# Performance work log

Measured on AMD Instinct MI355X. Metric: run time of the kernel, lower is better.

## Reference

```python
import jax, jax.numpy as jnp
import numpy as np

EPS = 1.1920929e-07  # torch.finfo(float32).eps, RMSNorm default eps

def _rms(x, w):
    return x * jax.lax.rsqrt(jnp.mean(x * x, axis=-1, keepdims=True) + EPS) * w

def setup_inputs() -> dict:
    key = jax.random.key(0)
    ks = jax.random.split(key, 8)
    V, E, M, L, B, T = 4096, 1024, 4096, 2, 32, 256
    s = 0.02
    return {
        "tokens": jax.random.randint(ks[0], (B, T), 0, V),
        "targets": jax.random.randint(ks[1], (B, T), 0, V),
        "emb_w": jax.random.normal(ks[2], (V, E), jnp.float32) * s,
        "block_norm_w": jax.random.normal(ks[3], (L, E), jnp.float32) * s,
        "fc1_w": jax.random.normal(ks[4], (L, M, E), jnp.float32) * s,
        "fc1_b": jnp.zeros((L, M), jnp.float32),
        "fc2_w": jax.random.normal(ks[5], (L, E, M), jnp.float32) * s,
        "fc2_b": jnp.zeros((L, E), jnp.float32),
        "norm_w": jax.random.normal(ks[6], (E,), jnp.float32) * s,
        "cur_w": jax.random.normal(ks[7], (E, E), jnp.float32) * s,
        "cur_b": jnp.zeros((E,), jnp.float32),
        "nxt_w": jax.random.normal(jax.random.fold_in(key, 99), (E, E), jnp.float32) * s,
        "nxt_b": jnp.zeros((E,), jnp.float32),
    }

def reference(tokens, targets, emb_w, block_norm_w, fc1_w, fc1_b, fc2_w, fc2_b,
              norm_w, cur_w, cur_b, nxt_w, nxt_b):
    B, T = tokens.shape
    E = emb_w.shape[1]
    L = block_norm_w.shape[0]
    embeds = emb_w[tokens]  # [B,T,E]

    def step(inp, xs):
        tok_emb, tok, tgt = xs  # [B,E], [B], [B]
        inp = tok_emb + inp
        h = inp
        for l in range(L):  # fixed small layer count
            y = jax.nn.silu(_rms(h, block_norm_w[l]) @ fc1_w[l].T + fc1_b[l])
            h = h + y @ fc2_w[l].T + fc2_b[l]
        x = _rms(inp + h, norm_w)
        cur_emb = x @ cur_w.T + cur_b
        nxt_emb = x @ nxt_w.T + nxt_b
        cur_logit = cur_emb @ emb_w.T  # [B,V]
        nxt_logit = nxt_emb @ emb_w.T
        lp_cur = jax.nn.log_softmax(cur_logit, axis=-1)
        lp_nxt = jax.nn.log_softmax(nxt_logit, axis=-1)
        ce_cur = -jnp.mean(jnp.take_along_axis(lp_cur, tok[:, None], axis=1))
        ce_nxt = -jnp.mean(jnp.take_along_axis(lp_nxt, tgt[:, None], axis=1))
        ce = (ce_cur + ce_nxt) / 2
        aux = jnp.mean((cur_emb - inp) ** 2)
        return nxt_emb, (nxt_logit, ce, aux)

    xs = (jnp.swapaxes(embeds, 0, 1), tokens.T, targets.T)
    init = jnp.zeros((B, E), embeds.dtype)
    _, (logits, ces, auxs) = jax.lax.scan(step, init, xs)
    return jnp.swapaxes(logits, 0, 1), jnp.mean(ces), jnp.mean(auxs)
```

## Files before the change

kernel.cpp:

```cpp
#include <hip/hip_runtime.h>
#include <math.h>

#define TT  256
#define BB  32
#define EE  1024
#define MM  4096
#define VV  4096
#define BE  (BB*EE)
#define NROWS (TT*BB)
#define EPSF 1.1920929e-07f

typedef _Float16 h2 __attribute__((ext_vector_type(2)));

__device__ inline float dot2f(h2 a, h2 b, float c) {
#if __has_builtin(__builtin_amdgcn_fdot2)
  return __builtin_amdgcn_fdot2(a, b, c, false);
#else
  return c + (float)a[0] * (float)b[0] + (float)a[1] * (float)b[1];
#endif
}

__device__ inline unsigned ldb_u32(const unsigned* p) {
  return __hip_atomic_load((unsigned*)p, __ATOMIC_RELAXED, __HIP_MEMORY_SCOPE_AGENT);
}
__device__ inline void stb_u32(unsigned* p, unsigned v) {
  __hip_atomic_store(p, v, __ATOMIC_RELAXED, __HIP_MEMORY_SCOPE_AGENT);
}
__device__ inline void stb_f32(float* p, float v) {
  __hip_atomic_store(p, v, __ATOMIC_RELAXED, __HIP_MEMORY_SCOPE_AGENT);
}

__device__ inline void gbar4(unsigned* cnt, int sidx) {
  __syncthreads();
  if (threadIdx.x == 0) {
    unsigned* base = cnt + (size_t)sidx * 17 * 32;
    unsigned* gp = base + (blockIdx.x & 15) * 32;
    unsigned* mp = base + 16 * 32;
    unsigned old = __hip_atomic_fetch_add(gp, 1u, __ATOMIC_RELAXED,
                                          __HIP_MEMORY_SCOPE_AGENT);
    if (old == 15u)
      __hip_atomic_fetch_add(mp, 1u, __ATOMIC_RELAXED, __HIP_MEMORY_SCOPE_AGENT);
    while (__hip_atomic_load(mp, __ATOMIC_RELAXED, __HIP_MEMORY_SCOPE_AGENT) < 16u)
      __builtin_amdgcn_s_sleep(1);
  }
  __syncthreads();
}

template<int NR>
__device__ float fc1like(int tid, int cu,
    const float* __restrict__ src, const float* __restrict__ scl,
    const h2* __restrict__ wl, h2* __restrict__ xs, float* __restrict__ red,
    float* __restrict__ ssrow,
    float* __restrict__ seedDst, const float* __restrict__ seedAdd,
    const float* __restrict__ seedBias) {
  const int b = tid & 31, kq = tid >> 5;
  const int sb = tid >> 4, se = (tid & 15) * 8;
  const int ep0 = (tid & 15) * 4;
  float ssacc = 0.f;
  float acc[NR];
#pragma unroll
  for (int m = 0; m < NR; ++m) acc[m] = 0.f;
  const int seedChunk = cu >> 5;
  const int seedOff = (cu & 1) * 4;
  const bool seeder = (seedDst != nullptr) && ((tid & 15) == ((cu & 31) >> 1));

  float4 v0, v1, c0v, c1v;
  auto ldchunk = [&](int c) {
    v0 = *(const float4*)&src[sb * EE + c * 128 + se];
    v1 = *(const float4*)&src[sb * EE + c * 128 + se + 4];
    c0v = *(const float4*)&scl[c * 128 + se];
    c1v = *(const float4*)&scl[c * 128 + se + 4];
  };
  auto flush = [&](int c) {
    h2* dst = xs + (c & 1) * (64 * 33);
    ssacc += v0.x*v0.x + v0.y*v0.y + v0.z*v0.z + v0.w*v0.w
           + v1.x*v1.x + v1.y*v1.y + v1.z*v1.z + v1.w*v1.w;
    h2 p0, p1, p2, p3;
    p0[0]=(_Float16)(v0.x*c0v.x); p0[1]=(_Float16)(v0.y*c0v.y);
    p1[0]=(_Float16)(v0.z*c0v.z); p1[1]=(_Float16)(v0.w*c0v.w);
    p2[0]=(_Float16)(v1.x*c1v.x); p2[1]=(_Float16)(v1.y*c1v.y);
    p3[0]=(_Float16)(v1.z*c1v.z); p3[1]=(_Float16)(v1.w*c1v.w);
    dst[(ep0+0)*33+sb]=p0; dst[(ep0+1)*33+sb]=p1;
    dst[(ep0+2)*33+sb]=p2; dst[(ep0+3)*33+sb]=p3;
    if (seeder && c == seedChunk) {
      const int e0 = c * 128 + se + seedOff;
      float a0, a1, a2, a3;
      if (seedOff == 0) { a0 = v0.x; a1 = v0.y; a2 = v0.z; a3 = v0.w; }
      else              { a0 = v1.x; a1 = v1.y; a2 = v1.z; a3 = v1.w; }
      float d0 = a0 + seedBias[e0 + 0];
      float d1 = a1 + seedBias[e0 + 1];
      float d2 = a2 + seedBias[e0 + 2];
      float d3 = a3 + seedBias[e0 + 3];
      if (seedAdd) {
        d0 += seedAdd[sb * EE + e0 + 0];
        d1 += seedAdd[sb * EE + e0 + 1];
        d2 += seedAdd[sb * EE + e0 + 2];
        d3 += seedAdd[sb * EE + e0 + 3];
      }
      stb_f32(&seedDst[sb * EE + e0 + 0], d0);
      stb_f32(&seedDst[sb * EE + e0 + 1], d1);
      stb_f32(&seedDst[sb * EE + e0 + 2], d2);
      stb_f32(&seedDst[sb * EE + e0 + 3], d3);
    }
  };
  ldchunk(0); flush(0);
  __syncthreads();
  for (int c = 0; c < 8; ++c) {
    if (c < 7) ldchunk(c + 1);
    const h2* xb = xs + (c & 1) * (64 * 33);
    h2 x0 = xb[(kq*4+0)*33+b], x1 = xb[(kq*4+1)*33+b],
       x2 = xb[(kq*4+2)*33+b], x3 = xb[(kq*4+3)*33+b];
#pragma unroll
    for (int m = 0; m < NR; ++m) {
      const h2* wp = &wl[m * 512 + c * 64 + kq * 4];
      float a = acc[m];
      a = dot2f(x0, wp[0], a); a = dot2f(x1, wp[1], a);
      a = dot2f(x2, wp[2], a); a = dot2f(x3, wp[3], a);
      acc[m] = a;
    }
    if (c < 7) flush(c + 1);
    __syncthreads();
  }
  ssacc += __shfl_xor(ssacc, 8);
  ssacc += __shfl_xor(ssacc, 4);
  ssacc += __shfl_xor(ssacc, 2);
  ssacc += __shfl_xor(ssacc, 1);
  if ((tid & 15) == 0) ssrow[sb] = ssacc;
#pragma unroll
  for (int m = 0; m < NR; ++m) acc[m] += __shfl_xor(acc[m], 32);
  const int wv = tid >> 6, ln = tid & 63;
  if (ln < 32) {
#pragma unroll
    for (int m = 0; m < NR; ++m) red[wv * 544 + ln * 17 + m] = acc[m];
  }
  __syncthreads();
  float z = 0.f;
  if (tid < 32 * NR) {
    const int b2 = (NR == 16) ? (tid >> 4) : (tid >> 2);
    const int m2 = tid & (NR - 1);
#pragma unroll
    for (int w = 0; w < 8; ++w) z += red[w * 544 + b2 * 17 + m2];
  }
  return z;
}

__device__ float fc2like(int tid,
    const unsigned* __restrict__ ysrc,
    const h2* __restrict__ wl, h2* __restrict__ xs, float* __restrict__ red) {
  const int b = tid & 31, kq = tid >> 5;
  const int sb = tid >> 4;
  const int ep0 = (tid & 15) * 4;
  float acc[16];
#pragma unroll
  for (int m = 0; m < 16; ++m) acc[m] = 0.f;
  unsigned q0, q1, q2, q3;
  auto ldchunk = [&](int c) {
    const unsigned* sp = ysrc + (size_t)sb * (MM / 2) + c * 64 + ep0;
    q0 = ldb_u32(sp + 0); q1 = ldb_u32(sp + 1);
    q2 = ldb_u32(sp + 2); q3 = ldb_u32(sp + 3);
  };
  auto flush = [&](int c) {
    h2* dst = xs + (c & 1) * (64 * 33);
    dst[(ep0+0)*33+sb] = __builtin_bit_cast(h2, q0);
    dst[(ep0+1)*33+sb] = __builtin_bit_cast(h2, q1);
    dst[(ep0+2)*33+sb] = __builtin_bit_cast(h2, q2);
    dst[(ep0+3)*33+sb] = __builtin_bit_cast(h2, q3);
  };
  ldchunk(0); flush(0);
  __syncthreads();
  for (int c = 0; c < 8; ++c) {
    if (c < 7) ldchunk(c + 1);
    const h2* xb = xs + (c & 1) * (64 * 33);
    h2 x0 = xb[(kq*4+0)*33+b], x1 = xb[(kq*4+1)*33+b],
       x2 = xb[(kq*4+2)*33+b], x3 = xb[(kq*4+3)*33+b];
#pragma unroll
    for (int m = 0; m < 16; ++m) {
      const h2* wp = &wl[m * 512 + c * 64 + kq * 4];
      float a = acc[m];
      a = dot2f(x0, wp[0], a); a = dot2f(x1, wp[1], a);
      a = dot2f(x2, wp[2], a); a = dot2f(x3, wp[3], a);
      acc[m] = a;
    }
    if (c < 7) flush(c + 1);
    __syncthreads();
  }
#pragma unroll
  for (int m = 0; m < 16; ++m) acc[m] += __shfl_xor(acc[m], 32);
  const int wv = tid >> 6, ln = tid & 63;
  if (ln < 32) {
#pragma unroll
    for (int m = 0; m < 16; ++m) red[wv * 544 + ln * 17 + m] = acc[m];
  }
  __syncthreads();
  const int b2 = tid >> 4, m2 = tid & 15;
  float z = 0.f;
#pragma unroll
  for (int w = 0; w < 8; ++w) z += red[w * 544 + b2 * 17 + m2];
  return z;
}

struct Scan4Params {
  const int* tokens; const float* embw;
  const float* bnw; const float* fc1w; const float* fc1b;
  const float* fc2w; const float* fc2b;
  const float* nw; const float* nxtw; const float* nxtb;
  float* inp_all;
  float* s_all;
  float* hbuf_all;
  float* nxt_all;
  unsigned* yh;
  float* ssS;
  unsigned* cnt;
};

__global__ __launch_bounds__(512, 1) void k_scan4(Scan4Params p) {
  extern __shared__ __align__(16) char smem[];
  h2* w1a = (h2*)smem;
  h2* w1b = (h2*)(smem + 32768);
  h2* w2a = (h2*)(smem + 65536);
  h2* w2b = (h2*)(smem + 98304);
  h2* wn  = (h2*)(smem + 131072);
  h2* xs  = (h2*)(smem + 139264);
  float* red = (float*)(smem + 139264);
  float* ssrow = (float*)(smem + 156672);
  const int tid = threadIdx.x;
  const int cu = blockIdx.x;
  const int cg = cu & 63, ks = cu >> 6;

#pragma unroll 4
  for (int r = 0; r < 16; ++r) {
    float2 f = *(const float2*)&p.fc1w[(size_t)(cu * 16 + r) * EE + tid * 2];
    h2 h; h[0] = (_Float16)f.x; h[1] = (_Float16)f.y;
    w1a[r * 512 + tid] = h;
    float2 g = *(const float2*)&p.fc1w[(size_t)MM * EE +
                                       (size_t)(cu * 16 + r) * EE + tid * 2];
    h2 hb; hb[0] = (_Float16)g.x; hb[1] = (_Float16)g.y;
    w1b[r * 512 + tid] = hb;
    float2 a = *(const float2*)&p.fc2w[(size_t)(cg * 16 + r) * MM +
                                       ks * 1024 + tid * 2];
    h2 ha; ha[0] = (_Float16)a.x; ha[1] = (_Float16)a.y;
    w2a[r * 512 + tid] = ha;
    float2 bb = *(const float2*)&p.fc2w[(size_t)EE * MM +
                                        (size_t)(cg * 16 + r) * MM +
                                        ks * 1024 + tid * 2];
    h2 hc; hc[0] = (_Float16)bb.x; hc[1] = (_Float16)bb.y;
    w2b[r * 512 + tid] = hc;
  }
#pragma unroll
  for (int r = 0; r < 4; ++r) {
    float2 f = *(const float2*)&p.nxtw[(size_t)(cu * 4 + r) * EE + tid * 2];
    h2 h; h[0] = (_Float16)f.x; h[1] = (_Float16)f.y;
    wn[r * 512 + tid] = h;
  }
  __syncthreads();

  int sidx = 0;
  for (int t = 0; t < TT; ++t) {
    const float* inp = p.inp_all + (size_t)t * BE;
    float* hb = p.hbuf_all + (size_t)t * BE;
    float* st = p.s_all + (size_t)t * BE;

    {
      float z = fc1like<16>(tid, cu, inp, p.bnw, w1a, xs, red, ssrow,
                            hb, nullptr, p.fc2b);
      const int b2 = tid >> 4, m2 = tid & 15, gm = cu * 16 + m2;
      float rinv = rsqrtf(ssrow[b2] * (1.f / EE) + EPSF);
      float zz = z * rinv + p.fc1b[gm];
      float yv = zz / (1.f + expf(-zz));
      unsigned bits = (unsigned)__builtin_bit_cast(unsigned short, (_Float16)yv);
      unsigned other = __shfl_xor(bits, 1);
      if ((tid & 1) == 0)
        stb_u32(&p.yh[b2 * (MM / 2) + (gm >> 1)], bits | (other << 16));
    }
    gbar4(p.cnt, sidx++);
    {
      float z = fc2like(tid, p.yh + ks * 512, w2a, xs, red);
      atomicAdd(&hb[(tid >> 4) * EE + cg * 16 + (tid & 15)], z);
    }
    gbar4(p.cnt, sidx++);
    {
      float z = fc1like<16>(tid, cu, hb, p.bnw + EE, w1b, xs, red, ssrow,
                            st, inp, p.fc2b + EE);
      const int b2 = tid >> 4, m2 = tid & 15, gm = cu * 16 + m2;
      float rinv = rsqrtf(ssrow[b2] * (1.f / EE) + EPSF);
      float zz = z * rinv + p.fc1b[MM + gm];
      float yv = zz / (1.f + expf(-zz));
      unsigned bits = (unsigned)__builtin_bit_cast(unsigned short, (_Float16)yv);
      unsigned other = __shfl_xor(bits, 1);
      if ((tid & 1) == 0)
        stb_u32(&p.yh[b2 * (MM / 2) + (gm >> 1)], bits | (other << 16));
    }
    gbar4(p.cnt, sidx++);
    {
      float z = fc2like(tid, p.yh + ks * 512, w2b, xs, red);
      atomicAdd(&st[(tid >> 4) * EE + cg * 16 + (tid & 15)], z);
    }
    gbar4(p.cnt, sidx++);
    {
      float z = fc1like<4>(tid, cu, st, p.nw, wn, xs, red, ssrow,
                           nullptr, nullptr, nullptr);
      if (cu == 0 && tid < 32) p.ssS[t * 32 + tid] = ssrow[tid];
      if (tid < 128) {
        const int b2 = tid >> 2, m2 = tid & 3, gn = cu * 4 + m2;
        float rinv = rsqrtf(ssrow[b2] * (1.f / EE) + EPSF);
        float nv = z * rinv + p.nxtb[gn];
        stb_f32(&p.nxt_all[(size_t)t * BE + b2 * EE + gn], nv);
        if (t + 1 < TT) {
          int tok = p.tokens[b2 * TT + t + 1];
          stb_f32(&p.inp_all[(size_t)(t + 1) * BE + b2 * EE + gn],
                  p.embw[(size_t)tok * EE + gn] + nv);
        }
      }
    }
    gbar4(p.cnt, sidx++);
  }
}


__global__ void k_zero(float* __restrict__ p, int n) {
  int i = blockIdx.x * 256 + threadIdx.x;
  if (i < n) p[i] = 0.f;
}

__global__ void k_init(const int* __restrict__ tokens,
                       const float* __restrict__ embw,
                       float* __restrict__ inp0) {
  int b = blockIdx.x;
  int tok = tokens[b * TT];
  int e = threadIdx.x * 4;
  float4 v = *(const float4*)&embw[(size_t)tok * EE + e];
  *(float4*)&inp0[b * EE + e] = v;
}


__global__ __launch_bounds__(256)
void k_fc1(const float* __restrict__ h, const float* __restrict__ bnw,
           const float* __restrict__ W, const float* __restrict__ bias,
           float* __restrict__ yout, float* __restrict__ initDst,
           const float* __restrict__ initAdd, const float* __restrict__ initBias) {
  __shared__ __align__(16) float Hs[32][68];
  __shared__ __align__(16) float Ws[8][68];
  __shared__ float ssrow[32];
  const int tid = threadIdx.x;
  const int col0 = blockIdx.x * 8;
  const int c = tid & 7;
  const int b = tid >> 3;
  const bool writer = (blockIdx.x == 0);
  float acc = 0.f;
  float ssl[8];
#pragma unroll
  for (int j = 0; j < 8; ++j) ssl[j] = 0.f;
  for (int kc = 0; kc < EE; kc += 64) {
#pragma unroll
    for (int j = 0; j < 8; ++j) {
      int i = tid + j * 256;
      int bb = i >> 6, k = i & 63;
      float v = h[bb * EE + kc + k];
      ssl[j] += v * v;
      Hs[bb][k] = v * bnw[kc + k];
      if (writer) {
        float d = v + initBias[kc + k];
        if (initAdd) d += initAdd[bb * EE + kc + k];
        initDst[bb * EE + kc + k] = d;
      }
    }
#pragma unroll
    for (int j = 0; j < 2; ++j) {
      int i = tid + j * 256;
      int cc = i >> 6, k = i & 63;
      Ws[cc][k] = W[(size_t)(col0 + cc) * EE + kc + k];
    }
    __syncthreads();
#pragma unroll
    for (int k = 0; k < 64; k += 4) {
      float4 w4 = *(const float4*)&Ws[c][k];
      float4 h4 = *(const float4*)&Hs[b][k];
      acc += h4.x * w4.x + h4.y * w4.y + h4.z * w4.z + h4.w * w4.w;
    }
    __syncthreads();
  }
  const int wv = tid >> 6;
#pragma unroll
  for (int j = 0; j < 8; ++j) {
    float v = ssl[j];
#pragma unroll
    for (int off = 32; off > 0; off >>= 1) v += __shfl_xor(v, off);
    if ((tid & 63) == 0) ssrow[wv + 4 * j] = v;
  }
  __syncthreads();
  float rinv = rsqrtf(ssrow[b] * (1.f / EE) + EPSF);
  float z = acc * rinv + bias[col0 + c];
  yout[b * MM + col0 + c] = z / (1.f + expf(-z));
}

__global__ __launch_bounds__(256)
void k_fc2(const float* __restrict__ y, const float* __restrict__ W2,
           float* __restrict__ dest) {
  __shared__ __align__(16) float Ys[32][68];
  __shared__ __align__(16) float Ws[16][68];
  const int tid = threadIdx.x;
  const int cgi = blockIdx.x & 63;
  const int ks = blockIdx.x >> 6;
  const int col0 = cgi * 16;
  const int c = tid & 15;
  const int bq = tid >> 4;
  float acc0 = 0.f, acc1 = 0.f;
  const int kend = ks * 512 + 512;
  for (int kc = ks * 512; kc < kend; kc += 64) {
#pragma unroll
    for (int j = 0; j < 8; ++j) {
      int i = tid + j * 256;
      int bb = i >> 6, k = i & 63;
      Ys[bb][k] = y[bb * MM + kc + k];
    }
#pragma unroll
    for (int j = 0; j < 4; ++j) {
      int i = tid + j * 256;
      int cc = i >> 6, k = i & 63;
      Ws[cc][k] = W2[(size_t)(col0 + cc) * MM + kc + k];
    }
    __syncthreads();
#pragma unroll
    for (int k = 0; k < 64; k += 4) {
      float4 w4 = *(const float4*)&Ws[c][k];
      float4 a4 = *(const float4*)&Ys[bq][k];
      float4 b4 = *(const float4*)&Ys[bq + 16][k];
      acc0 += a4.x * w4.x + a4.y * w4.y + a4.z * w4.z + a4.w * w4.w;
      acc1 += b4.x * w4.x + b4.y * w4.y + b4.z * w4.z + b4.w * w4.w;
    }
    __syncthreads();
  }
  atomicAdd(&dest[bq * EE + col0 + c], acc0);
  atomicAdd(&dest[(bq + 16) * EE + col0 + c], acc1);
}

__global__ __launch_bounds__(256)
void k_nxt(const float* __restrict__ s, const float* __restrict__ nw,
           const float* __restrict__ Wn, const float* __restrict__ nb,
           float* __restrict__ nxt_out, float* __restrict__ ss_out,
           const int* __restrict__ tokens, const float* __restrict__ embw,
           float* __restrict__ inp_next, int tnext) {
  __shared__ __align__(16) float Xs[32][68];
  __shared__ __align__(16) float Ws[8][68];
  __shared__ float ssrow[32];
  const int tid = threadIdx.x;
  const int col0 = blockIdx.x * 8;
  const int c = tid & 7;
  const int b = tid >> 3;
  float acc = 0.f;
  float ssl[8];
#pragma unroll
  for (int j = 0; j < 8; ++j) ssl[j] = 0.f;
  for (int kc = 0; kc < EE; kc += 64) {
#pragma unroll
    for (int j = 0; j < 8; ++j) {
      int i = tid + j * 256;
      int bb = i >> 6, k = i & 63;
      float v = s[bb * EE + kc + k];
      ssl[j] += v * v;
      Xs[bb][k] = v * nw[kc + k];
    }
#pragma unroll
    for (int j = 0; j < 2; ++j) {
      int i = tid + j * 256;
      int cc = i >> 6, k = i & 63;
      Ws[cc][k] = Wn[(size_t)(col0 + cc) * EE + kc + k];
    }
    __syncthreads();
#pragma unroll
    for (int k = 0; k < 64; k += 4) {
      float4 w4 = *(const float4*)&Ws[c][k];
      float4 h4 = *(const float4*)&Xs[b][k];
      acc += h4.x * w4.x + h4.y * w4.y + h4.z * w4.z + h4.w * w4.w;
    }
    __syncthreads();
  }
  const int wv = tid >> 6;
#pragma unroll
  for (int j = 0; j < 8; ++j) {
    float v = ssl[j];
#pragma unroll
    for (int off = 32; off > 0; off >>= 1) v += __shfl_xor(v, off);
    if ((tid & 63) == 0) {
      ssrow[wv + 4 * j] = v;
      if (blockIdx.x == 0) ss_out[wv + 4 * j] = v;
    }
  }
  __syncthreads();
  float rinv = rsqrtf(ssrow[b] * (1.f / EE) + EPSF);
  float nv = acc * rinv + nb[col0 + c];
  nxt_out[b * EE + col0 + c] = nv;
  if (inp_next) {
    int tok = tokens[b * TT + tnext];
    inp_next[b * EE + col0 + c] = embw[(size_t)tok * EE + col0 + c] + nv;
  }
}


__global__ __launch_bounds__(256)
void k_curemb(const float* __restrict__ s_all, const float* __restrict__ ss_s,
              const float* __restrict__ nw, const float* __restrict__ Wc,
              const float* __restrict__ cb, const float* __restrict__ inp_all,
              float* __restrict__ cur_out, float* __restrict__ aux_accum) {
  __shared__ __align__(16) h2 Ah[8 * 68];
  __shared__ __align__(16) h2 Bh[8 * 68];
  __shared__ float rr[64];
  __shared__ float wred[4];
  const int tid = threadIdx.x;
  const int rt = blockIdx.x & 127;
  const int ct = blockIdx.x >> 7;
  const int row0 = rt * 64, col0 = ct * 64;
  if (tid < 64) rr[tid] = rsqrtf(ss_s[row0 + tid] * (1.f / EE) + EPSF);
  __syncthreads();
  float acc[4][4];
#pragma unroll
  for (int i = 0; i < 4; ++i)
#pragma unroll
    for (int j = 0; j < 4; ++j) acc[i][j] = 0.f;
  const int tx = tid & 15, ty = tid >> 4;
  for (int kc = 0; kc < EE; kc += 16) {
#pragma unroll
    for (int j = 0; j < 2; ++j) {
      int idx = tid + j * 256;
      int kp = idx & 7, m = idx >> 3;
      float2 f = *(const float2*)&s_all[(size_t)(row0 + m) * EE + kc + 2 * kp];
      float2 n2 = *(const float2*)&nw[kc + 2 * kp];
      float r = rr[m];
      h2 hv; hv[0] = (_Float16)(f.x * r * n2.x); hv[1] = (_Float16)(f.y * r * n2.y);
      Ah[kp * 68 + m] = hv;
      float2 w2 = *(const float2*)&Wc[(size_t)(col0 + m) * EE + kc + 2 * kp];
      h2 hw; hw[0] = (_Float16)w2.x; hw[1] = (_Float16)w2.y;
      Bh[kp * 68 + m] = hw;
    }
    __syncthreads();
#pragma unroll
    for (int kp = 0; kp < 8; ++kp) {
      h2 a0 = Ah[kp*68 + tx*4 + 0], a1 = Ah[kp*68 + tx*4 + 1];
      h2 a2 = Ah[kp*68 + tx*4 + 2], a3 = Ah[kp*68 + tx*4 + 3];
      h2 b0 = Bh[kp*68 + ty*4 + 0], b1 = Bh[kp*68 + ty*4 + 1];
      h2 b2 = Bh[kp*68 + ty*4 + 2], b3 = Bh[kp*68 + ty*4 + 3];
      acc[0][0]=dot2f(a0,b0,acc[0][0]); acc[0][1]=dot2f(a0,b1,acc[0][1]);
      acc[0][2]=dot2f(a0,b2,acc[0][2]); acc[0][3]=dot2f(a0,b3,acc[0][3]);
      acc[1][0]=dot2f(a1,b0,acc[1][0]); acc[1][1]=dot2f(a1,b1,acc[1][1]);
      acc[1][2]=dot2f(a1,b2,acc[1][2]); acc[1][3]=dot2f(a1,b3,acc[1][3]);
      acc[2][0]=dot2f(a2,b0,acc[2][0]); acc[2][1]=dot2f(a2,b1,acc[2][1]);
      acc[2][2]=dot2f(a2,b2,acc[2][2]); acc[2][3]=dot2f(a2,b3,acc[2][3]);
      acc[3][0]=dot2f(a3,b0,acc[3][0]); acc[3][1]=dot2f(a3,b1,acc[3][1]);
      acc[3][2]=dot2f(a3,b2,acc[3][2]); acc[3][3]=dot2f(a3,b3,acc[3][3]);
    }
    __syncthreads();
  }
  float auxp = 0.f;
#pragma unroll
  for (int i = 0; i < 4; ++i) {
    int r = row0 + tx * 4 + i;
#pragma unroll
    for (int j = 0; j < 4; ++j) {
      int col = col0 + ty * 4 + j;
      float v = acc[i][j] + cb[col];
      cur_out[(size_t)r * EE + col] = v;
      float d = v - inp_all[(size_t)r * EE + col];
      auxp += d * d;
    }
  }
#pragma unroll
  for (int off = 32; off > 0; off >>= 1) auxp += __shfl_xor(auxp, off);
  if ((tid & 63) == 0) wred[tid >> 6] = auxp;
  __syncthreads();
  if (tid == 0) atomicAdd(aux_accum, wred[0] + wred[1] + wred[2] + wred[3]);
}

__global__ __launch_bounds__(256)
void k_logits(const float* __restrict__ A, const float* __restrict__ embw,
              const int* __restrict__ idxs, float* __restrict__ rowsum,
              float* __restrict__ lidx, float* __restrict__ store) {
  __shared__ __align__(16) h2 Ah[8 * 68];
  __shared__ __align__(16) h2 Bh[8 * 68];
  __shared__ float rowpart[64];
  const int tid = threadIdx.x;
  const int rt = blockIdx.x & 127;
  const int ct = blockIdx.x >> 7;
  const int row0 = rt * 64, col0 = ct * 64;
  float acc[4][4];
#pragma unroll
  for (int i = 0; i < 4; ++i)
#pragma unroll
    for (int j = 0; j < 4; ++j) acc[i][j] = 0.f;
  const int tx = tid & 15, ty = tid >> 4;
  for (int kc = 0; kc < EE; kc += 16) {
#pragma unroll
    for (int j = 0; j < 2; ++j) {
      int idx = tid + j * 256;
      int kp = idx & 7, m = idx >> 3;
      float2 f = *(const float2*)&A[(size_t)(row0 + m) * EE + kc + 2 * kp];
      h2 hv; hv[0] = (_Float16)f.x; hv[1] = (_Float16)f.y;
      Ah[kp * 68 + m] = hv;
      float2 w2 = *(const float2*)&embw[(size_t)(col0 + m) * EE + kc + 2 * kp];
      h2 hw; hw[0] = (_Float16)w2.x; hw[1] = (_Float16)w2.y;
      Bh[kp * 68 + m] = hw;
    }
    __syncthreads();
#pragma unroll
    for (int kp = 0; kp < 8; ++kp) {
      h2 a0 = Ah[kp*68 + tx*4 + 0], a1 = Ah[kp*68 + tx*4 + 1];
      h2 a2 = Ah[kp*68 + tx*4 + 2], a3 = Ah[kp*68 + tx*4 + 3];
      h2 b0 = Bh[kp*68 + ty*4 + 0], b1 = Bh[kp*68 + ty*4 + 1];
      h2 b2 = Bh[kp*68 + ty*4 + 2], b3 = Bh[kp*68 + ty*4 + 3];
      acc[0][0]=dot2f(a0,b0,acc[0][0]); acc[0][1]=dot2f(a0,b1,acc[0][1]);
      acc[0][2]=dot2f(a0,b2,acc[0][2]); acc[0][3]=dot2f(a0,b3,acc[0][3]);
      acc[1][0]=dot2f(a1,b0,acc[1][0]); acc[1][1]=dot2f(a1,b1,acc[1][1]);
      acc[1][2]=dot2f(a1,b2,acc[1][2]); acc[1][3]=dot2f(a1,b3,acc[1][3]);
      acc[2][0]=dot2f(a2,b0,acc[2][0]); acc[2][1]=dot2f(a2,b1,acc[2][1]);
      acc[2][2]=dot2f(a2,b2,acc[2][2]); acc[2][3]=dot2f(a2,b3,acc[2][3]);
      acc[3][0]=dot2f(a3,b0,acc[3][0]); acc[3][1]=dot2f(a3,b1,acc[3][1]);
      acc[3][2]=dot2f(a3,b2,acc[3][2]); acc[3][3]=dot2f(a3,b3,acc[3][3]);
    }
    __syncthreads();
  }
  if (tid < 64) rowpart[tid] = 0.f;
  __syncthreads();
#pragma unroll
  for (int i = 0; i < 4; ++i) {
    int r = row0 + tx * 4 + i;
    int t = r >> 5, bb = r & 31;
    int idx = idxs[bb * TT + t];
    float e0 = expf(acc[i][0]);
    float e1 = expf(acc[i][1]);
    float e2 = expf(acc[i][2]);
    float e3 = expf(acc[i][3]);
    atomicAdd(&rowpart[tx * 4 + i], e0 + e1 + e2 + e3);
    int cbase = col0 + ty * 4;
#pragma unroll
    for (int j = 0; j < 4; ++j)
      if (cbase + j == idx) lidx[r] = acc[i][j];
    if (store) {
      float4 o = make_float4(acc[i][0], acc[i][1], acc[i][2], acc[i][3]);
      *(float4*)(store + ((size_t)bb * TT + t) * VV + cbase) = o;
    }
  }
  __syncthreads();
  if (tid < 64) atomicAdd(&rowsum[row0 + tid], rowpart[tid]);
}

__global__ void k_final(const float* __restrict__ rs_cur,
                        const float* __restrict__ rs_nxt,
                        const float* __restrict__ ltok,
                        const float* __restrict__ ltgt,
                        const float* __restrict__ aux_accum,
                        float* __restrict__ out) {
  float p = 0.f;
  for (int r = threadIdx.x; r < NROWS; r += 256)
    p += (ltok[r] - logf(rs_cur[r])) + (ltgt[r] - logf(rs_nxt[r]));
#pragma unroll
  for (int off = 32; off > 0; off >>= 1) p += __shfl_xor(p, off);
  __shared__ float w[4];
  if ((threadIdx.x & 63) == 0) w[threadIdx.x >> 6] = p;
  __syncthreads();
  if (threadIdx.x == 0) {
    float tot = w[0] + w[1] + w[2] + w[3];
    out[0] = -tot / (2.f * (float)NROWS);
    out[1] = aux_accum[0] * (1.f / ((float)NROWS * EE));
  }
}


extern "C" void kernel_launch(void* const* d_in, const int* in_sizes, int n_in,
                              void* d_out, int out_size, void* d_ws, size_t ws_size,
                              hipStream_t stream) {
  (void)in_sizes; (void)n_in; (void)out_size; (void)ws_size;
  const int*   tokens  = (const int*)d_in[0];
  const int*   targets = (const int*)d_in[1];
  const float* embw    = (const float*)d_in[2];
  const float* bnw     = (const float*)d_in[3];
  const float* fc1w    = (const float*)d_in[4];
  const float* fc1b    = (const float*)d_in[5];
  const float* fc2w    = (const float*)d_in[6];
  const float* fc2b    = (const float*)d_in[7];
  const float* nw      = (const float*)d_in[8];
  const float* curw    = (const float*)d_in[9];
  const float* curb    = (const float*)d_in[10];
  const float* nxtw    = (const float*)d_in[11];
  const float* nxtb    = (const float*)d_in[12];
  float* out = (float*)d_out;

  float* cur_all  = out;
  float* s_all    = out + (size_t)NROWS * EE;
  float* inp_all  = out + 2 * (size_t)NROWS * EE;
  float* hbuf_all = out + 3 * (size_t)NROWS * EE;

  float* ws       = (float*)d_ws;
  float* nxt_all  = ws;
  float* ltok     = ws + 8388608;
  float* ltgt     = ws + 8396800;
  unsigned* yh    = (unsigned*)(ws + 8404992);
  float* rs_cur   = ws + 8470528;
  float* rs_nxt   = ws + 8478720;
  float* auxac    = ws + 8486912;
  unsigned* cnt   = (unsigned*)(ws + 8486944);
  float* ssS      = ws + 9183264;
  float* ybuf     = ws + 9191456;

  const int nzero = (8486944 + 696320) - 8470528;
  k_zero<<<(nzero + 255) / 256, 256, 0, stream>>>(rs_cur, nzero);
  k_init<<<32, 256, 0, stream>>>(tokens, embw, inp_all);

  Scan4Params p;
  p.tokens = tokens; p.embw = embw; p.bnw = bnw;
  p.fc1w = fc1w; p.fc1b = fc1b; p.fc2w = fc2w; p.fc2b = fc2b;
  p.nw = nw; p.nxtw = nxtw; p.nxtb = nxtb;
  p.inp_all = inp_all; p.s_all = s_all; p.hbuf_all = hbuf_all;
  p.nxt_all = nxt_all; p.yh = yh; p.ssS = ssS; p.cnt = cnt;

  const size_t shmem = 156800;
  hipError_t err = hipFuncSetAttribute((const void*)k_scan4,
      hipFuncAttributeMaxDynamicSharedMemorySize, (int)shmem);
  if (err == hipSuccess) {
    void* args[] = { &p };
    err = hipLaunchCooperativeKernel((const void*)k_scan4, dim3(256), dim3(512),
                                     args, shmem, stream);
  }
  if (err != hipSuccess) {
    float* hbuf = hbuf_all;
    for (int t = 0; t < TT; ++t) {
      const float* inp = inp_all + (size_t)t * BE;
      float* s = s_all + (size_t)t * BE;
      k_fc1<<<512, 256, 0, stream>>>(inp, bnw, fc1w, fc1b, ybuf,
                                     hbuf, nullptr, fc2b);
      k_fc2<<<512, 256, 0, stream>>>(ybuf, fc2w, hbuf);
      k_fc1<<<512, 256, 0, stream>>>(hbuf, bnw + EE, fc1w + (size_t)MM * EE,
                                     fc1b + MM, ybuf, s, inp, fc2b + EE);
      k_fc2<<<512, 256, 0, stream>>>(ybuf, fc2w + (size_t)EE * MM, s);
      k_nxt<<<128, 256, 0, stream>>>(s, nw, nxtw, nxtb,
                                     nxt_all + (size_t)t * BE, ssS + t * BB,
                                     tokens, embw,
                                     (t + 1 < TT) ? inp_all + (size_t)(t + 1) * BE : nullptr,
                                     t + 1);
    }
  }

  k_curemb<<<2048, 256, 0, stream>>>(s_all, ssS, nw, curw, curb, inp_all,
                                     cur_all, auxac);
  k_logits<<<8192, 256, 0, stream>>>(cur_all, embw, tokens, rs_cur, ltok, nullptr);
  k_logits<<<8192, 256, 0, stream>>>(nxt_all, embw, targets, rs_nxt, ltgt, out);
  k_final<<<1, 256, 0, stream>>>(rs_cur, rs_nxt, ltok, ltgt, auxac,
                                 out + (size_t)NROWS * VV);
}
```

Before: 17.34 ms.

## Double scan block to 1024 threads and reduce partial sums via LDS atomics

The persistent cooperative scan kernel now runs 1024 threads per block instead of 512, so each thread handles half as much of the K dimension in the fc1/fc2-style matvecs and half as much of the input staging. The per-wave partial-sum buffer, previously summed over 8 wave slots, is replaced by shared-memory atomicAdd into one zeroed buffer placed outside the staging area. The aim is more waves in flight to hide latency within each serial timestep and a shorter reduction tail. In exchange, the register budget per thread is halved, LDS atomics can contend, and half the threads sit idle in the epilogues.

```diff
diff --git a/kernel.cpp b/kernel.cpp
--- a/kernel.cpp
+++ b/kernel.cpp
@@ -54,43 +54,35 @@
     float* __restrict__ seedDst, const float* __restrict__ seedAdd,
     const float* __restrict__ seedBias) {
   const int b = tid & 31, kq = tid >> 5;
-  const int sb = tid >> 4, se = (tid & 15) * 8;
-  const int ep0 = (tid & 15) * 4;
+  const int sb = tid >> 5, ln = tid & 31;
+  const int e2 = ln * 2;
   float ssacc = 0.f;
   float acc[NR];
 #pragma unroll
   for (int m = 0; m < NR; ++m) acc[m] = 0.f;
   const int seedChunk = cu >> 5;
-  const int seedOff = (cu & 1) * 4;
-  const bool seeder = (seedDst != nullptr) && ((tid & 15) == ((cu & 31) >> 1));
-
-  float4 v0, v1, c0v, c1v;
+  const bool seeder = (seedDst != nullptr) && (ln == (cu & 31));
+
+  for (int i = tid; i < 544; i += 1024) red[i] = 0.f;
+
+  float4 v0, c0v;
   auto ldchunk = [&](int c) {
-    v0 = *(const float4*)&src[sb * EE + c * 128 + se];
-    v1 = *(const float4*)&src[sb * EE + c * 128 + se + 4];
-    c0v = *(const float4*)&scl[c * 128 + se];
-    c1v = *(const float4*)&scl[c * 128 + se + 4];
+    v0 = *(const float4*)&src[sb * EE + c * 128 + ln * 4];
+    c0v = *(const float4*)&scl[c * 128 + ln * 4];
   };
   auto flush = [&](int c) {
     h2* dst = xs + (c & 1) * (64 * 33);
-    ssacc += v0.x*v0.x + v0.y*v0.y + v0.z*v0.z + v0.w*v0.w
-           + v1.x*v1.x + v1.y*v1.y + v1.z*v1.z + v1.w*v1.w;
-    h2 p0, p1, p2, p3;
+    ssacc += v0.x*v0.x + v0.y*v0.y + v0.z*v0.z + v0.w*v0.w;
+    h2 p0, p1;
     p0[0]=(_Float16)(v0.x*c0v.x); p0[1]=(_Float16)(v0.y*c0v.y);
     p1[0]=(_Float16)(v0.z*c0v.z); p1[1]=(_Float16)(v0.w*c0v.w);
-    p2[0]=(_Float16)(v1.x*c1v.x); p2[1]=(_Float16)(v1.y*c1v.y);
-    p3[0]=(_Float16)(v1.z*c1v.z); p3[1]=(_Float16)(v1.w*c1v.w);
-    dst[(ep0+0)*33+sb]=p0; dst[(ep0+1)*33+sb]=p1;
-    dst[(ep0+2)*33+sb]=p2; dst[(ep0+3)*33+sb]=p3;
+    dst[(e2+0)*33+sb]=p0; dst[(e2+1)*33+sb]=p1;
     if (seeder && c == seedChunk) {
-      const int e0 = c * 128 + se + seedOff;
-      float a0, a1, a2, a3;
-      if (seedOff == 0) { a0 = v0.x; a1 = v0.y; a2 = v0.z; a3 = v0.w; }
-      else              { a0 = v1.x; a1 = v1.y; a2 = v1.z; a3 = v1.w; }
-      float d0 = a0 + seedBias[e0 + 0];
-      float d1 = a1 + seedBias[e0 + 1];
-      float d2 = a2 + seedBias[e0 + 2];
-      float d3 = a3 + seedBias[e0 + 3];
+      const int e0 = c * 128 + ln * 4;
+      float d0 = v0.x + seedBias[e0 + 0];
+      float d1 = v0.y + seedBias[e0 + 1];
+      float d2 = v0.z + seedBias[e0 + 2];
+      float d3 = v0.w + seedBias[e0 + 3];
       if (seedAdd) {
         d0 += seedAdd[sb * EE + e0 + 0];
         d1 += seedAdd[sb * EE + e0 + 1];
@@ -108,38 +100,34 @@
   for (int c = 0; c < 8; ++c) {
     if (c < 7) ldchunk(c + 1);
     const h2* xb = xs + (c & 1) * (64 * 33);
-    h2 x0 = xb[(kq*4+0)*33+b], x1 = xb[(kq*4+1)*33+b],
-       x2 = xb[(kq*4+2)*33+b], x3 = xb[(kq*4+3)*33+b];
+    h2 x0 = xb[(kq*2+0)*33+b], x1 = xb[(kq*2+1)*33+b];
 #pragma unroll
     for (int m = 0; m < NR; ++m) {
-      const h2* wp = &wl[m * 512 + c * 64 + kq * 4];
+      const h2* wp = &wl[m * 512 + c * 64 + kq * 2];
       float a = acc[m];
       a = dot2f(x0, wp[0], a); a = dot2f(x1, wp[1], a);
-      a = dot2f(x2, wp[2], a); a = dot2f(x3, wp[3], a);
       acc[m] = a;
     }
     if (c < 7) flush(c + 1);
     __syncthreads();
   }
+  ssacc += __shfl_xor(ssacc, 16);
   ssacc += __shfl_xor(ssacc, 8);
   ssacc += __shfl_xor(ssacc, 4);
   ssacc += __shfl_xor(ssacc, 2);
   ssacc += __shfl_xor(ssacc, 1);
-  if ((tid & 15) == 0) ssrow[sb] = ssacc;
+  if (ln == 0) ssrow[sb] = ssacc;
 #pragma unroll
   for (int m = 0; m < NR; ++m) acc[m] += __shfl_xor(acc[m], 32);
-  const int wv = tid >> 6, ln = tid & 63;
-  if (ln < 32) {
-#pragma unroll
-    for (int m = 0; m < NR; ++m) red[wv * 544 + ln * 17 + m] = acc[m];
+  if ((tid & 63) < 32) {
+#pragma unroll
+    for (int m = 0; m < NR; ++m) atomicAdd(&red[b * 17 + m], acc[m]);
   }
   __syncthreads();
   float z = 0.f;
   if (tid < 32 * NR) {
-    const int b2 = (NR == 16) ? (tid >> 4) : (tid >> 2);
-    const int m2 = tid & (NR - 1);
-#pragma unroll
-    for (int w = 0; w < 8; ++w) z += red[w * 544 + b2 * 17 + m2];
+    const int b2 = tid / NR, m2 = tid % NR;
+    z = red[b2 * 17 + m2];
   }
   return z;
 }
@@ -148,37 +136,33 @@
     const unsigned* __restrict__ ysrc,
     const h2* __restrict__ wl, h2* __restrict__ xs, float* __restrict__ red) {
   const int b = tid & 31, kq = tid >> 5;
-  const int sb = tid >> 4;
-  const int ep0 = (tid & 15) * 4;
+  const int sb = tid >> 5, ln = tid & 31;
+  const int e2 = ln * 2;
   float acc[16];
 #pragma unroll
   for (int m = 0; m < 16; ++m) acc[m] = 0.f;
-  unsigned q0, q1, q2, q3;
+  for (int i = tid; i < 544; i += 1024) red[i] = 0.f;
+  unsigned q0, q1;
   auto ldchunk = [&](int c) {
-    const unsigned* sp = ysrc + (size_t)sb * (MM / 2) + c * 64 + ep0;
+    const unsigned* sp = ysrc + (size_t)sb * (MM / 2) + c * 64 + ln * 2;
     q0 = ldb_u32(sp + 0); q1 = ldb_u32(sp + 1);
-    q2 = ldb_u32(sp + 2); q3 = ldb_u32(sp + 3);
   };
   auto flush = [&](int c) {
     h2* dst = xs + (c & 1) * (64 * 33);
-    dst[(ep0+0)*33+sb] = __builtin_bit_cast(h2, q0);
-    dst[(ep0+1)*33+sb] = __builtin_bit_cast(h2, q1);
-    dst[(ep0+2)*33+sb] = __builtin_bit_cast(h2, q2);
-    dst[(ep0+3)*33+sb] = __builtin_bit_cast(h2, q3);
+    dst[(e2+0)*33+sb] = __builtin_bit_cast(h2, q0);
+    dst[(e2+1)*33+sb] = __builtin_bit_cast(h2, q1);
   };
   ldchunk(0); flush(0);
   __syncthreads();
   for (int c = 0; c < 8; ++c) {
     if (c < 7) ldchunk(c + 1);
     const h2* xb = xs + (c & 1) * (64 * 33);
-    h2 x0 = xb[(kq*4+0)*33+b], x1 = xb[(kq*4+1)*33+b],
-       x2 = xb[(kq*4+2)*33+b], x3 = xb[(kq*4+3)*33+b];
+    h2 x0 = xb[(kq*2+0)*33+b], x1 = xb[(kq*2+1)*33+b];
 #pragma unroll
     for (int m = 0; m < 16; ++m) {
-      const h2* wp = &wl[m * 512 + c * 64 + kq * 4];
+      const h2* wp = &wl[m * 512 + c * 64 + kq * 2];
       float a = acc[m];
       a = dot2f(x0, wp[0], a); a = dot2f(x1, wp[1], a);
-      a = dot2f(x2, wp[2], a); a = dot2f(x3, wp[3], a);
       acc[m] = a;
     }
     if (c < 7) flush(c + 1);
@@ -186,16 +170,16 @@
   }
 #pragma unroll
   for (int m = 0; m < 16; ++m) acc[m] += __shfl_xor(acc[m], 32);
-  const int wv = tid >> 6, ln = tid & 63;
-  if (ln < 32) {
-#pragma unroll
-    for (int m = 0; m < 16; ++m) red[wv * 544 + ln * 17 + m] = acc[m];
-  }
-  __syncthreads();
-  const int b2 = tid >> 4, m2 = tid & 15;
+  if ((tid & 63) < 32) {
+#pragma unroll
+    for (int m = 0; m < 16; ++m) atomicAdd(&red[b * 17 + m], acc[m]);
+  }
+  __syncthreads();
   float z = 0.f;
-#pragma unroll
-  for (int w = 0; w < 8; ++w) z += red[w * 544 + b2 * 17 + m2];
+  if (tid < 512) {
+    const int b2 = tid >> 4, m2 = tid & 15;
+    z = red[b2 * 17 + m2];
+  }
   return z;
 }
 
@@ -213,7 +197,7 @@
   unsigned* cnt;
 };
 
-__global__ __launch_bounds__(512, 1) void k_scan4(Scan4Params p) {
+__global__ __launch_bounds__(1024, 1) void k_scan4(Scan4Params p) {
   extern __shared__ __align__(16) char smem[];
   h2* w1a = (h2*)smem;
   h2* w1b = (h2*)(smem + 32768);
@@ -221,36 +205,40 @@
   h2* w2b = (h2*)(smem + 98304);
   h2* wn  = (h2*)(smem + 131072);
   h2* xs  = (h2*)(smem + 139264);
-  float* red = (float*)(smem + 139264);
-  float* ssrow = (float*)(smem + 156672);
+  float* red = (float*)(smem + 156160);
+  float* ssrow = (float*)(smem + 158336);
   const int tid = threadIdx.x;
   const int cu = blockIdx.x;
   const int cg = cu & 63, ks = cu >> 6;
 
-#pragma unroll 4
-  for (int r = 0; r < 16; ++r) {
-    float2 f = *(const float2*)&p.fc1w[(size_t)(cu * 16 + r) * EE + tid * 2];
+#pragma unroll
+  for (int j = 0; j < 8; ++j) {
+    int idx = tid + j * 1024;
+    int r = idx >> 9, k = idx & 511;
+    float2 f = *(const float2*)&p.fc1w[(size_t)(cu * 16 + r) * EE + k * 2];
     h2 h; h[0] = (_Float16)f.x; h[1] = (_Float16)f.y;
-    w1a[r * 512 + tid] = h;
+    w1a[r * 512 + k] = h;
     float2 g = *(const float2*)&p.fc1w[(size_t)MM * EE +
-                                       (size_t)(cu * 16 + r) * EE + tid * 2];
+                                       (size_t)(cu * 16 + r) * EE + k * 2];
     h2 hb; hb[0] = (_Float16)g.x; hb[1] = (_Float16)g.y;
-    w1b[r * 512 + tid] = hb;
+    w1b[r * 512 + k] = hb;
     float2 a = *(const float2*)&p.fc2w[(size_t)(cg * 16 + r) * MM +
-                                       ks * 1024 + tid * 2];
+                                       ks * 1024 + k * 2];
     h2 ha; ha[0] = (_Float16)a.x; ha[1] = (_Float16)a.y;
-    w2a[r * 512 + tid] = ha;
+    w2a[r * 512 + k] = ha;
     float2 bb = *(const float2*)&p.fc2w[(size_t)EE * MM +
                                         (size_t)(cg * 16 + r) * MM +
-                                        ks * 1024 + tid * 2];
+                                        ks * 1024 + k * 2];
     h2 hc; hc[0] = (_Float16)bb.x; hc[1] = (_Float16)bb.y;
-    w2b[r * 512 + tid] = hc;
-  }
-#pragma unroll
-  for (int r = 0; r < 4; ++r) {
-    float2 f = *(const float2*)&p.nxtw[(size_t)(cu * 4 + r) * EE + tid * 2];
+    w2b[r * 512 + k] = hc;
+  }
+#pragma unroll
+  for (int j = 0; j < 2; ++j) {
+    int idx = tid + j * 1024;
+    int r = idx >> 9, k = idx & 511;
+    float2 f = *(const float2*)&p.nxtw[(size_t)(cu * 4 + r) * EE + k * 2];
     h2 h; h[0] = (_Float16)f.x; h[1] = (_Float16)f.y;
-    wn[r * 512 + tid] = h;
+    wn[r * 512 + k] = h;
   }
   __syncthreads();
 
@@ -263,37 +251,43 @@
     {
       float z = fc1like<16>(tid, cu, inp, p.bnw, w1a, xs, red, ssrow,
                             hb, nullptr, p.fc2b);
-      const int b2 = tid >> 4, m2 = tid & 15, gm = cu * 16 + m2;
-      float rinv = rsqrtf(ssrow[b2] * (1.f / EE) + EPSF);
-      float zz = z * rinv + p.fc1b[gm];
-      float yv = zz / (1.f + expf(-zz));
-      unsigned bits = (unsigned)__builtin_bit_cast(unsigned short, (_Float16)yv);
-      unsigned other = __shfl_xor(bits, 1);
-      if ((tid & 1) == 0)
-        stb_u32(&p.yh[b2 * (MM / 2) + (gm >> 1)], bits | (other << 16));
+      if (tid < 512) {
+        const int b2 = tid >> 4, m2 = tid & 15, gm = cu * 16 + m2;
+        float rinv = rsqrtf(ssrow[b2] * (1.f / EE) + EPSF);
+        float zz = z * rinv + p.fc1b[gm];
+        float yv = zz / (1.f + expf(-zz));
+        unsigned bits = (unsigned)__builtin_bit_cast(unsigned short, (_Float16)yv);
+        unsigned other = __shfl_xor(bits, 1);
+        if ((tid & 1) == 0)
+          stb_u32(&p.yh[b2 * (MM / 2) + (gm >> 1)], bits | (other << 16));
+      }
     }
     gbar4(p.cnt, sidx++);
     {
       float z = fc2like(tid, p.yh + ks * 512, w2a, xs, red);
-      atomicAdd(&hb[(tid >> 4) * EE + cg * 16 + (tid & 15)], z);
+      if (tid < 512)
+        atomicAdd(&hb[(tid >> 4) * EE + cg * 16 + (tid & 15)], z);
     }
     gbar4(p.cnt, sidx++);
     {
       float z = fc1like<16>(tid, cu, hb, p.bnw + EE, w1b, xs, red, ssrow,
                             st, inp, p.fc2b + EE);
-      const int b2 = tid >> 4, m2 = tid & 15, gm = cu * 16 + m2;
-      float rinv = rsqrtf(ssrow[b2] * (1.f / EE) + EPSF);
-      float zz = z * rinv + p.fc1b[MM + gm];
-      float yv = zz / (1.f + expf(-zz));
-      unsigned bits = (unsigned)__builtin_bit_cast(unsigned short, (_Float16)yv);
-      unsigned other = __shfl_xor(bits, 1);
-      if ((tid & 1) == 0)
-        stb_u32(&p.yh[b2 * (MM / 2) + (gm >> 1)], bits | (other << 16));
+      if (tid < 512) {
+        const int b2 = tid >> 4, m2 = tid & 15, gm = cu * 16 + m2;
+        float rinv = rsqrtf(ssrow[b2] * (1.f / EE) + EPSF);
+        float zz = z * rinv + p.fc1b[MM + gm];
+        float yv = zz / (1.f + expf(-zz));
+        unsigned bits = (unsigned)__builtin_bit_cast(unsigned short, (_Float16)yv);
+        unsigned other = __shfl_xor(bits, 1);
+        if ((tid & 1) == 0)
+          stb_u32(&p.yh[b2 * (MM / 2) + (gm >> 1)], bits | (other << 16));
+      }
     }
     gbar4(p.cnt, sidx++);
     {
       float z = fc2like(tid, p.yh + ks * 512, w2b, xs, red);
-      atomicAdd(&st[(tid >> 4) * EE + cg * 16 + (tid & 15)], z);
+      if (tid < 512)
+        atomicAdd(&st[(tid >> 4) * EE + cg * 16 + (tid & 15)], z);
     }
     gbar4(p.cnt, sidx++);
     {
@@ -711,12 +705,12 @@
   p.inp_all = inp_all; p.s_all = s_all; p.hbuf_all = hbuf_all;
   p.nxt_all = nxt_all; p.yh = yh; p.ssS = ssS; p.cnt = cnt;
 
-  const size_t shmem = 156800;
+  const size_t shmem = 158464;
   hipError_t err = hipFuncSetAttribute((const void*)k_scan4,
       hipFuncAttributeMaxDynamicSharedMemorySize, (int)shmem);
   if (err == hipSuccess) {
     void* args[] = { &p };
-    err = hipLaunchCooperativeKernel((const void*)k_scan4, dim3(256), dim3(512),
+    err = hipLaunchCooperativeKernel((const void*)k_scan4, dim3(256), dim3(1024),
                                      args, shmem, stream);
   }
   if (err != hipSuccess) {
```

Result: slower. 46.34 ms (+167.3%).
